# Optimization experiments

Hardware: AMD Instinct MI355X
Metric: run time of the kernel (lower is better)

The kernel has to match this reference:

```python
import jax, jax.numpy as jnp
import numpy as np

NUM_HEADS = 12
HEAD_DIM = 64
SCALE = HEAD_DIM ** -0.5


def setup_inputs() -> dict:
    key = jax.random.key(0)
    k1, k2, k3, k4, k5 = jax.random.split(key, 5)
    B, N, C = 4, 2048, NUM_HEADS * HEAD_DIM
    x = jax.random.normal(k1, (B, N, C), dtype=jnp.float32)
    W_qkv = jax.random.normal(k2, (C, 3 * C), dtype=jnp.float32) * (C ** -0.5)
    b_qkv = jax.random.normal(k3, (3 * C,), dtype=jnp.float32) * 0.02
    W_proj = jax.random.normal(k4, (C, C), dtype=jnp.float32) * (C ** -0.5)
    b_proj = jax.random.normal(k5, (C,), dtype=jnp.float32) * 0.02
    return {"x": x, "W_qkv": W_qkv, "b_qkv": b_qkv, "W_proj": W_proj, "b_proj": b_proj}


def reference(x, W_qkv, b_qkv, W_proj, b_proj):
    B, N, C = x.shape
    H, D = NUM_HEADS, HEAD_DIM
    qkv = x @ W_qkv + b_qkv                      # [B, N, 3C]
    qkv = qkv.reshape(B, N, 3, H, D)
    q = qkv[:, :, 0].transpose(0, 2, 1, 3) * SCALE  # [B, H, N, D]
    k = qkv[:, :, 1].transpose(0, 2, 1, 3)          # [B, H, N, D]
    v = qkv[:, :, 2].transpose(0, 2, 1, 3)          # [B, H, N, D]
    attn = jnp.einsum("bhnd,bhmd->bhnm", q, k)   # [B, H, N, N]
    attn = jax.nn.softmax(attn, axis=-1)
    ctx = jnp.einsum("bhnm,bhmd->bhnd", attn, v)  # [B, H, N, D]
    attn_out = ctx.transpose(0, 2, 1, 3).reshape(B, N, C)
    out = attn_out @ W_proj + b_proj
    return (out, attn_out)
```

## Files before the change

kernel.cpp:

```cpp
#include <hip/hip_runtime.h>
#include <stdint.h>

typedef unsigned short u16;
using bf16x8 = __attribute__((ext_vector_type(8))) __bf16;
using s16x8  = __attribute__((ext_vector_type(8))) short;
using f32x4  = __attribute__((ext_vector_type(4))) float;

#define SCALE_Q 0.125f
#define LOG2E 1.44269504088896f

__device__ __forceinline__ u16 f2bf(float f) {
  union { float f; uint32_t u; } v; v.f = f;
  uint32_t u = v.u;
  return (u16)((u + 0x7FFFu + ((u >> 16) & 1)) >> 16);
}

__device__ __forceinline__ bf16x8 ld_frag(const u16* p) {
  return __builtin_bit_cast(bf16x8, *(const s16x8*)p);
}

__device__ __forceinline__ f32x4 MF(bf16x8 a, bf16x8 b, f32x4 c) {
  return __builtin_amdgcn_mfma_f32_16x16x32_bf16(a, b, c, 0, 0, 0);
}

__device__ __forceinline__ void gld16(const u16* g, u16* l) {
  __builtin_amdgcn_global_load_lds(
      (const __attribute__((address_space(1))) uint32_t*)g,
      (__attribute__((address_space(3))) uint32_t*)l, 16, 0, 0);
}

__device__ __forceinline__ uint32_t pk_bf16(float a, float b) {
  uint32_t u0 = __builtin_bit_cast(uint32_t, a) + 0x8000u;
  uint32_t u1 = __builtin_bit_cast(uint32_t, b) + 0x8000u;
  return __builtin_amdgcn_perm(u1, u0, 0x07060302u);
}

__global__ void cvt_f32_bf16(const float* __restrict__ in, u16* __restrict__ out, int n) {
  int i = (blockIdx.x * 256 + threadIdx.x) * 4;
  if (i < n) {
    float4 v = *(const float4*)(in + i);
    uint2 o;
    o.x = (uint32_t)f2bf(v.x) | ((uint32_t)f2bf(v.y) << 16);
    o.y = (uint32_t)f2bf(v.z) | ((uint32_t)f2bf(v.w) << 16);
    *(uint2*)(out + i) = o;
  }
}

__global__ void transpose_cvt(const float* __restrict__ in, u16* __restrict__ out, int R, int C) {
  __shared__ float tile[32][33];
  int c0 = blockIdx.x * 32, r0 = blockIdx.y * 32;
  int tx = threadIdx.x & 31, ty = threadIdx.x >> 5;
#pragma unroll
  for (int j = 0; j < 32; j += 8)
    tile[ty + j][tx] = in[(size_t)(r0 + ty + j) * C + c0 + tx];
  __syncthreads();
#pragma unroll
  for (int j = 0; j < 32; j += 8)
    out[(size_t)(c0 + ty + j) * R + r0 + tx] = f2bf(tile[tx][ty + j]);
}

template <int MODE>
__global__ __launch_bounds__(256) void gemm_k768(
    const u16* __restrict__ A, const u16* __restrict__ Bt, const float* __restrict__ bias,
    u16* __restrict__ q_out, u16* __restrict__ k_out, u16* __restrict__ v_out,
    float* __restrict__ c_out) {
  constexpr int K = 768;
  __shared__ __align__(16) u16 sA[128 * 64];
  __shared__ __align__(16) u16 sB[128 * 64];
  const int tid = threadIdx.x;
  const int lane = tid & 63, wave = tid >> 6;
  const int ml = lane & 15, kg = lane >> 4;
  const int wr = wave >> 1, wc = wave & 1;
  const int bn = blockIdx.x, bm = blockIdx.y;

  f32x4 acc[4][4] = {};
  const u16* Abase = A + (size_t)(bm * 128) * K;
  const u16* Bbase = Bt + (size_t)(bn * 128) * K;

  for (int k0 = 0; k0 < K; k0 += 64) {
#pragma unroll
    for (int p = 0; p < 4; p++) {
      int q = p * 256 + tid;
      int r = q >> 3, s = q & 7, c = s ^ (r & 7);
      gld16(Abase + (size_t)r * K + k0 + c * 8, sA + q * 8);
      gld16(Bbase + (size_t)r * K + k0 + c * 8, sB + q * 8);
    }
    __syncthreads();
#pragma unroll
    for (int kc = 0; kc < 2; kc++) {
      bf16x8 af[4], bfr[4];
      int ac = kc * 4 + kg;
#pragma unroll
      for (int i = 0; i < 4; i++) {
        int arow = wr * 64 + i * 16 + ml;
        af[i] = ld_frag(sA + (arow * 8 + (ac ^ (arow & 7))) * 8);
        int brow = wc * 64 + i * 16 + ml;
        bfr[i] = ld_frag(sB + (brow * 8 + (ac ^ (brow & 7))) * 8);
      }
#pragma unroll
      for (int mi = 0; mi < 4; mi++)
#pragma unroll
        for (int ni = 0; ni < 4; ni++)
          acc[mi][ni] = MF(af[mi], bfr[ni], acc[mi][ni]);
    }
    __syncthreads();
  }

  if (MODE == 0) {
#pragma unroll
    for (int ni = 0; ni < 4; ni++) {
      int n = bn * 128 + wc * 64 + ni * 16 + ml;
      int s = n / 768, rem = n - s * 768;
      int h = rem >> 6, d = rem & 63;
      float bv = bias[n];
      if (s == 2) {
#pragma unroll
        for (int mi = 0; mi < 4; mi++) {
          int m0 = bm * 128 + wr * 64 + mi * 16 + kg * 4;
          int bi = m0 >> 11, tok = m0 & 2047;
          uint2 o;
          o.x = pk_bf16(acc[mi][ni][0] + bv, acc[mi][ni][1] + bv);
          o.y = pk_bf16(acc[mi][ni][2] + bv, acc[mi][ni][3] + bv);
          *(uint2*)&v_out[((size_t)(bi * 12 + h) * 64 + d) * 2048 + tok] = o;
        }
      } else {
        u16* dst = (s == 0) ? q_out : k_out;
        float scl = (s == 0) ? SCALE_Q * LOG2E : 1.0f;
#pragma unroll
        for (int mi = 0; mi < 4; mi++) {
          int m0 = bm * 128 + wr * 64 + mi * 16 + kg * 4;
#pragma unroll
          for (int r = 0; r < 4; r++) {
            int m = m0 + r;
            int bi = m >> 11, tok = m & 2047;
            dst[(size_t)(bi * 12 + h) * 131072 + (size_t)tok * 64 + d] = f2bf((acc[mi][ni][r] + bv) * scl);
          }
        }
      }
    }
  } else {
#pragma unroll
    for (int ni = 0; ni < 4; ni++) {
      int n = bn * 128 + wc * 64 + ni * 16 + ml;
      float bv = bias[n];
#pragma unroll
      for (int mi = 0; mi < 4; mi++) {
        int m0 = bm * 128 + wr * 64 + mi * 16 + kg * 4;
#pragma unroll
        for (int r = 0; r < 4; r++)
          c_out[(size_t)(m0 + r) * 768 + n] = acc[mi][ni][r] + bv;
      }
    }
  }
}

__global__ __launch_bounds__(256) void gemm_proj(
    const u16* __restrict__ A, const u16* __restrict__ Bt, const float* __restrict__ bias,
    float* __restrict__ c_out) {
  constexpr int K = 768;
  __shared__ __align__(16) u16 sA[128 * 64];
  __shared__ __align__(16) u16 sB[64 * 64];
  const int tid = threadIdx.x;
  const int lane = tid & 63, wave = tid >> 6;
  const int ml = lane & 15, kg = lane >> 4;
  const int bn = blockIdx.x, bm = blockIdx.y;
  f32x4 acc[2][4] = {};
  const u16* Abase = A + (size_t)(bm * 128) * K;
  const u16* Bbase = Bt + (size_t)(bn * 64) * K;

  for (int k0 = 0; k0 < K; k0 += 64) {
#pragma unroll
    for (int p = 0; p < 4; p++) {
      int q = p * 256 + tid;
      int r = q >> 3, s = q & 7, c = s ^ (r & 7);
      gld16(Abase + (size_t)r * K + k0 + c * 8, sA + q * 8);
    }
#pragma unroll
    for (int p = 0; p < 2; p++) {
      int q = p * 256 + tid;
      int r = q >> 3, s = q & 7, c = s ^ (r & 7);
      gld16(Bbase + (size_t)r * K + k0 + c * 8, sB + q * 8);
    }
    __syncthreads();
#pragma unroll
    for (int kc = 0; kc < 2; kc++) {
      int ac = kc * 4 + kg;
      bf16x8 af[2], bfr[4];
#pragma unroll
      for (int i = 0; i < 2; i++) {
        int arow = wave * 32 + i * 16 + ml;
        af[i] = ld_frag(sA + (arow * 8 + (ac ^ (arow & 7))) * 8);
      }
#pragma unroll
      for (int i = 0; i < 4; i++) {
        int brow = i * 16 + ml;
        bfr[i] = ld_frag(sB + (brow * 8 + (ac ^ (brow & 7))) * 8);
      }
#pragma unroll
      for (int mi = 0; mi < 2; mi++)
#pragma unroll
        for (int ni = 0; ni < 4; ni++)
          acc[mi][ni] = MF(af[mi], bfr[ni], acc[mi][ni]);
    }
    __syncthreads();
  }
#pragma unroll
  for (int ni = 0; ni < 4; ni++) {
    int n = bn * 64 + ni * 16 + ml;
    float bv = bias[n];
#pragma unroll
    for (int mi = 0; mi < 2; mi++) {
      int m0 = bm * 128 + wave * 32 + mi * 16 + kg * 4;
#pragma unroll
      for (int r = 0; r < 4; r++)
        c_out[(size_t)(m0 + r) * 768 + n] = acc[mi][ni][r] + bv;
    }
  }
}

__global__ __launch_bounds__(256, 3) void attn_kernel(
    const u16* __restrict__ qs, const u16* __restrict__ ks, const u16* __restrict__ vt,
    float* __restrict__ attn_f32, u16* __restrict__ attn_bf) {
  __shared__ __align__(16) u16 sK[2][64 * 64];
  __shared__ __align__(16) u16 sV[2][64 * 64];
  __shared__ __align__(16) u16 sP[4][32 * 72];
  const int tid = threadIdx.x, lane = tid & 63, wave = tid >> 6;
  const int ml = lane & 15, kg = lane >> 4;
  const int bh = blockIdx.y;
  const int q0 = blockIdx.x * 128 + wave * 32;
  const size_t base = (size_t)bh * 2048 * 64;

  bf16x8 qf[2][2];
#pragma unroll
  for (int qt = 0; qt < 2; qt++) {
    const u16* qp = qs + base + (size_t)(q0 + qt * 16 + ml) * 64 + kg * 8;
    qf[qt][0] = ld_frag(qp);
    qf[qt][1] = ld_frag(qp + 32);
  }
  f32x4 l4[2] = {};
  f32x4 O[2][4] = {};
  u16* myP = sP[wave];

  int buf = 0;
  auto stage = [&](int b, int kt) {
#pragma unroll
    for (int p = 0; p < 2; p++) {
      int q = p * 256 + tid;
      int r = q >> 3, s = q & 7, c = s ^ (r & 7);
      gld16(ks + base + (size_t)(kt + r) * 64 + c * 8, &sK[b][q * 8]);
      gld16(vt + base + (size_t)r * 2048 + kt + c * 8, &sV[b][q * 8]);
    }
  };

  stage(0, 0);
  for (int kt = 0; kt < 2048; kt += 64) {
    __syncthreads();
    if (kt + 64 < 2048) stage(buf ^ 1, kt + 64);

    f32x4 sc[2][4] = {};
#pragma unroll
    for (int nt = 0; nt < 4; nt++) {
#pragma unroll
      for (int kc = 0; kc < 2; kc++) {
        int krow = nt * 16 + ml;
        int c = kc * 4 + kg;
        bf16x8 kf = ld_frag(&sK[buf][(krow * 8 + (c ^ (krow & 7))) * 8]);
        sc[0][nt] = MF(kf, qf[0][kc], sc[0][nt]);
        sc[1][nt] = MF(kf, qf[1][kc], sc[1][nt]);
      }
    }

#pragma unroll
    for (int qt = 0; qt < 2; qt++) {
      u16* rowp = myP + (qt * 16 + ml) * 72;
#pragma unroll
      for (int nt = 0; nt < 4; nt++) {
        f32x4 p;
#pragma unroll
        for (int r = 0; r < 4; r++) p[r] = __builtin_amdgcn_exp2f(sc[qt][nt][r]);
        l4[qt] += p;
        uint2 w;
        w.x = pk_bf16(p[0], p[1]);
        w.y = pk_bf16(p[2], p[3]);
        *(uint2*)(rowp + nt * 16 + kg * 4) = w;
      }
    }

    asm volatile("s_waitcnt lgkmcnt(0)" ::: "memory");

#pragma unroll
    for (int kc = 0; kc < 2; kc++) {
      bf16x8 pf0 = ld_frag(myP + ml * 72 + kc * 32 + kg * 8);
      bf16x8 pf1 = ld_frag(myP + (16 + ml) * 72 + kc * 32 + kg * 8);
#pragma unroll
      for (int nt2 = 0; nt2 < 4; nt2++) {
        int vrow = nt2 * 16 + ml;
        int c = kc * 4 + kg;
        bf16x8 vf = ld_frag(&sV[buf][(vrow * 8 + (c ^ (vrow & 7))) * 8]);
        O[0][nt2] = MF(pf0, vf, O[0][nt2]);
        O[1][nt2] = MF(pf1, vf, O[1][nt2]);
      }
    }
    buf ^= 1;
  }

  float linv[2];
#pragma unroll
  for (int qt = 0; qt < 2; qt++) {
    float s = l4[qt][0] + l4[qt][1] + l4[qt][2] + l4[qt][3];
    s += __shfl_xor(s, 16);
    s += __shfl_xor(s, 32);
    linv[qt] = __builtin_amdgcn_rcpf(s);
  }
  int b = bh / 12, h = bh - b * 12;
#pragma unroll
  for (int qt = 0; qt < 2; qt++)
#pragma unroll
    for (int r = 0; r < 4; r++) {
      float inv = __shfl(linv[qt], kg * 4 + r, 64);
      int qrow = q0 + qt * 16 + kg * 4 + r;
      size_t rowoff = ((size_t)(b * 2048 + qrow)) * 768 + h * 64;
#pragma unroll
      for (int nt2 = 0; nt2 < 4; nt2++) {
        float v = O[qt][nt2][r] * inv;
        int d = nt2 * 16 + ml;
        attn_f32[rowoff + d] = v;
        attn_bf[rowoff + d] = f2bf(v);
      }
    }
}

extern "C" void kernel_launch(void* const* d_in, const int* in_sizes, int n_in,
                              void* d_out, int out_size, void* d_ws, size_t ws_size,
                              hipStream_t stream) {
  const float* x      = (const float*)d_in[0];
  const float* W_qkv  = (const float*)d_in[1];
  const float* b_qkv  = (const float*)d_in[2];
  const float* W_proj = (const float*)d_in[3];
  const float* b_proj = (const float*)d_in[4];
  float* out      = (float*)d_out;
  float* attn_out = out + (size_t)8192 * 768;

  char* ws = (char*)d_ws;
  const size_t SZ_XB = (size_t)8192 * 768 * 2;
  u16* xb      = (u16*)(ws);
  u16* wqkv_t  = (u16*)(ws + SZ_XB);
  u16* wproj_t = (u16*)(ws + SZ_XB + 3538944);
  u16* qs      = (u16*)(ws + SZ_XB + 3538944 + 1179648);
  u16* ks      = (u16*)((char*)qs + SZ_XB);
  u16* vt      = (u16*)((char*)ks + SZ_XB);
  u16* ab      = xb;

  cvt_f32_bf16<<<6144, 256, 0, stream>>>(x, xb, 8192 * 768);
  transpose_cvt<<<dim3(2304 / 32, 768 / 32), 256, 0, stream>>>(W_qkv, wqkv_t, 768, 2304);
  transpose_cvt<<<dim3(768 / 32, 768 / 32), 256, 0, stream>>>(W_proj, wproj_t, 768, 768);
  gemm_k768<0><<<dim3(2304 / 128, 8192 / 128), 256, 0, stream>>>(
      xb, wqkv_t, b_qkv, qs, ks, vt, nullptr);
  attn_kernel<<<dim3(16, 48), 256, 0, stream>>>(qs, ks, vt, attn_out, ab);
  gemm_proj<<<dim3(12, 64), 256, 0, stream>>>(ab, wproj_t, b_proj, out);
}
```

Before: 231.5 us.

## Keep P in registers for PV MFMA and stage V-transpose stores through LDS

The attention kernel drops the per-wave LDS round trip for the softmax probabilities. It packs P directly into registers and computes O^T with the 16x16x16 bf16 MFMA, using V^T fragments as the A operand, so the output lands row-contiguous and can be written with vectorized float4/uint2 stores. The QKV GEMM epilogue for V blocks now transposes through shared memory so the V^T output is written with 16-byte row-contiguous stores instead of scattered 8-byte ones. The trade is more, smaller MFMAs (16x16x16 instead of 16x16x32) in exchange for removing the LDS write/wait/read traffic and uncoalesced epilogue stores.

```diff
diff --git a/kernel.cpp b/kernel.cpp
--- a/kernel.cpp
+++ b/kernel.cpp
@@ -4,6 +4,7 @@
 typedef unsigned short u16;
 using bf16x8 = __attribute__((ext_vector_type(8))) __bf16;
 using s16x8  = __attribute__((ext_vector_type(8))) short;
+using s16x4  = __attribute__((ext_vector_type(4))) short;
 using f32x4  = __attribute__((ext_vector_type(4))) float;
 
 #define SCALE_Q 0.125f
@@ -21,6 +22,9 @@
 
 __device__ __forceinline__ f32x4 MF(bf16x8 a, bf16x8 b, f32x4 c) {
   return __builtin_amdgcn_mfma_f32_16x16x32_bf16(a, b, c, 0, 0, 0);
+}
+__device__ __forceinline__ f32x4 MF16(s16x4 a, s16x4 b, f32x4 c) {
+  return __builtin_amdgcn_mfma_f32_16x16x16bf16_1k(a, b, c, 0, 0, 0);
 }
 
 __device__ __forceinline__ void gld16(const u16* g, u16* l) {
@@ -59,14 +63,13 @@
     out[(size_t)(c0 + ty + j) * R + r0 + tx] = f2bf(tile[tx][ty + j]);
 }
 
-template <int MODE>
-__global__ __launch_bounds__(256) void gemm_k768(
+__global__ __launch_bounds__(256) void gemm_qkv(
     const u16* __restrict__ A, const u16* __restrict__ Bt, const float* __restrict__ bias,
-    u16* __restrict__ q_out, u16* __restrict__ k_out, u16* __restrict__ v_out,
-    float* __restrict__ c_out) {
+    u16* __restrict__ q_out, u16* __restrict__ k_out, u16* __restrict__ v_out) {
   constexpr int K = 768;
-  __shared__ __align__(16) u16 sA[128 * 64];
-  __shared__ __align__(16) u16 sB[128 * 64];
+  __shared__ __align__(16) u16 smem[17408];
+  u16* sA = smem;
+  u16* sB = smem + 8192;
   const int tid = threadIdx.x;
   const int lane = tid & 63, wave = tid >> 6;
   const int ml = lane & 15, kg = lane >> 4;
@@ -106,49 +109,48 @@
     __syncthreads();
   }
 
-  if (MODE == 0) {
+  if (bn >= 12) {
+    uint32_t* t32 = (uint32_t*)smem;
+#pragma unroll
+    for (int ni = 0; ni < 4; ni++) {
+      int n_local = wc * 64 + ni * 16 + ml;
+      float bv = bias[bn * 128 + n_local];
+#pragma unroll
+      for (int mi = 0; mi < 4; mi++) {
+        int mh = wr * 32 + mi * 8 + kg * 2;
+        t32[n_local * 68 + mh]     = pk_bf16(acc[mi][ni][0] + bv, acc[mi][ni][1] + bv);
+        t32[n_local * 68 + mh + 1] = pk_bf16(acc[mi][ni][2] + bv, acc[mi][ni][3] + bv);
+      }
+    }
+    __syncthreads();
+    int row = tid >> 1, seg = tid & 1;
+    int dg = (bn - 12) * 128 + row;
+    int h = dg >> 6, d = dg & 63;
+    int bi = bm >> 4, tok0 = (bm & 15) * 128;
+    u16* dst = v_out + ((size_t)(bi * 12 + h) * 64 + d) * 2048 + tok0 + seg * 64;
+    const uint32_t* src = t32 + row * 68 + seg * 32;
+#pragma unroll
+    for (int j = 0; j < 8; j++)
+      *(uint4*)(dst + j * 8) = *(const uint4*)(src + j * 4);
+  } else {
 #pragma unroll
     for (int ni = 0; ni < 4; ni++) {
       int n = bn * 128 + wc * 64 + ni * 16 + ml;
-      int s = n / 768, rem = n - s * 768;
+      int s = n >> 9 >= 1 ? (n >= 768 ? 1 : 0) : 0;
+      int rem = n - s * 768;
       int h = rem >> 6, d = rem & 63;
       float bv = bias[n];
-      if (s == 2) {
-#pragma unroll
-        for (int mi = 0; mi < 4; mi++) {
-          int m0 = bm * 128 + wr * 64 + mi * 16 + kg * 4;
-          int bi = m0 >> 11, tok = m0 & 2047;
-          uint2 o;
-          o.x = pk_bf16(acc[mi][ni][0] + bv, acc[mi][ni][1] + bv);
-          o.y = pk_bf16(acc[mi][ni][2] + bv, acc[mi][ni][3] + bv);
-          *(uint2*)&v_out[((size_t)(bi * 12 + h) * 64 + d) * 2048 + tok] = o;
-        }
-      } else {
-        u16* dst = (s == 0) ? q_out : k_out;
-        float scl = (s == 0) ? SCALE_Q * LOG2E : 1.0f;
-#pragma unroll
-        for (int mi = 0; mi < 4; mi++) {
-          int m0 = bm * 128 + wr * 64 + mi * 16 + kg * 4;
-#pragma unroll
-          for (int r = 0; r < 4; r++) {
-            int m = m0 + r;
-            int bi = m >> 11, tok = m & 2047;
-            dst[(size_t)(bi * 12 + h) * 131072 + (size_t)tok * 64 + d] = f2bf((acc[mi][ni][r] + bv) * scl);
-          }
-        }
-      }
-    }
-  } else {
-#pragma unroll
-    for (int ni = 0; ni < 4; ni++) {
-      int n = bn * 128 + wc * 64 + ni * 16 + ml;
-      float bv = bias[n];
+      u16* dst = (s == 0) ? q_out : k_out;
+      float scl = (s == 0) ? SCALE_Q * LOG2E : 1.0f;
 #pragma unroll
       for (int mi = 0; mi < 4; mi++) {
         int m0 = bm * 128 + wr * 64 + mi * 16 + kg * 4;
 #pragma unroll
-        for (int r = 0; r < 4; r++)
-          c_out[(size_t)(m0 + r) * 768 + n] = acc[mi][ni][r] + bv;
+        for (int r = 0; r < 4; r++) {
+          int m = m0 + r;
+          int bi = m >> 11, tok = m & 2047;
+          dst[(size_t)(bi * 12 + h) * 131072 + (size_t)tok * 64 + d] = f2bf((acc[mi][ni][r] + bv) * scl);
+        }
       }
     }
   }
@@ -223,7 +225,6 @@
     float* __restrict__ attn_f32, u16* __restrict__ attn_bf) {
   __shared__ __align__(16) u16 sK[2][64 * 64];
   __shared__ __align__(16) u16 sV[2][64 * 64];
-  __shared__ __align__(16) u16 sP[4][32 * 72];
   const int tid = threadIdx.x, lane = tid & 63, wave = tid >> 6;
   const int ml = lane & 15, kg = lane >> 4;
   const int bh = blockIdx.y;
@@ -239,7 +240,6 @@
   }
   f32x4 l4[2] = {};
   f32x4 O[2][4] = {};
-  u16* myP = sP[wave];
 
   int buf = 0;
   auto stage = [&](int b, int kt) {
@@ -270,9 +270,9 @@
       }
     }
 
-#pragma unroll
-    for (int qt = 0; qt < 2; qt++) {
-      u16* rowp = myP + (qt * 16 + ml) * 72;
+    s16x4 pb[2][4];
+#pragma unroll
+    for (int qt = 0; qt < 2; qt++)
 #pragma unroll
       for (int nt = 0; nt < 4; nt++) {
         f32x4 p;
@@ -282,52 +282,44 @@
         uint2 w;
         w.x = pk_bf16(p[0], p[1]);
         w.y = pk_bf16(p[2], p[3]);
-        *(uint2*)(rowp + nt * 16 + kg * 4) = w;
-      }
-    }
-
-    asm volatile("s_waitcnt lgkmcnt(0)" ::: "memory");
-
-#pragma unroll
-    for (int kc = 0; kc < 2; kc++) {
-      bf16x8 pf0 = ld_frag(myP + ml * 72 + kc * 32 + kg * 8);
-      bf16x8 pf1 = ld_frag(myP + (16 + ml) * 72 + kc * 32 + kg * 8);
-#pragma unroll
-      for (int nt2 = 0; nt2 < 4; nt2++) {
-        int vrow = nt2 * 16 + ml;
-        int c = kc * 4 + kg;
-        bf16x8 vf = ld_frag(&sV[buf][(vrow * 8 + (c ^ (vrow & 7))) * 8]);
-        O[0][nt2] = MF(pf0, vf, O[0][nt2]);
-        O[1][nt2] = MF(pf1, vf, O[1][nt2]);
+        pb[qt][nt] = __builtin_bit_cast(s16x4, w);
+      }
+
+#pragma unroll
+    for (int dt = 0; dt < 4; dt++) {
+      int r = dt * 16 + ml;
+#pragma unroll
+      for (int kc4 = 0; kc4 < 4; kc4++) {
+        int c0 = kc4 * 2 + (kg >> 1);
+        s16x4 vf = *(const s16x4*)(&sV[buf][((r * 8 + (c0 ^ (r & 7))) * 8 + (kg & 1) * 4)]);
+        O[0][dt] = MF16(vf, pb[0][kc4], O[0][dt]);
+        O[1][dt] = MF16(vf, pb[1][kc4], O[1][dt]);
       }
     }
     buf ^= 1;
   }
 
-  float linv[2];
+  int b = bh / 12, h = bh - b * 12;
 #pragma unroll
   for (int qt = 0; qt < 2; qt++) {
     float s = l4[qt][0] + l4[qt][1] + l4[qt][2] + l4[qt][3];
     s += __shfl_xor(s, 16);
     s += __shfl_xor(s, 32);
-    linv[qt] = __builtin_amdgcn_rcpf(s);
-  }
-  int b = bh / 12, h = bh - b * 12;
-#pragma unroll
-  for (int qt = 0; qt < 2; qt++)
-#pragma unroll
-    for (int r = 0; r < 4; r++) {
-      float inv = __shfl(linv[qt], kg * 4 + r, 64);
-      int qrow = q0 + qt * 16 + kg * 4 + r;
-      size_t rowoff = ((size_t)(b * 2048 + qrow)) * 768 + h * 64;
-#pragma unroll
-      for (int nt2 = 0; nt2 < 4; nt2++) {
-        float v = O[qt][nt2][r] * inv;
-        int d = nt2 * 16 + ml;
-        attn_f32[rowoff + d] = v;
-        attn_bf[rowoff + d] = f2bf(v);
-      }
-    }
+    float inv = __builtin_amdgcn_rcpf(s);
+    int qrow = q0 + qt * 16 + ml;
+    size_t rowoff = ((size_t)(b * 2048 + qrow)) * 768 + h * 64;
+#pragma unroll
+    for (int dt = 0; dt < 4; dt++) {
+      f32x4 v = O[qt][dt];
+      float4 o4 = {v[0] * inv, v[1] * inv, v[2] * inv, v[3] * inv};
+      int d0 = dt * 16 + kg * 4;
+      *(float4*)(attn_f32 + rowoff + d0) = o4;
+      uint2 w;
+      w.x = pk_bf16(o4.x, o4.y);
+      w.y = pk_bf16(o4.z, o4.w);
+      *(uint2*)(attn_bf + rowoff + d0) = w;
+    }
+  }
 }
 
 extern "C" void kernel_launch(void* const* d_in, const int* in_sizes, int n_in,
@@ -354,8 +346,7 @@
   cvt_f32_bf16<<<6144, 256, 0, stream>>>(x, xb, 8192 * 768);
   transpose_cvt<<<dim3(2304 / 32, 768 / 32), 256, 0, stream>>>(W_qkv, wqkv_t, 768, 2304);
   transpose_cvt<<<dim3(768 / 32, 768 / 32), 256, 0, stream>>>(W_proj, wproj_t, 768, 768);
-  gemm_k768<0><<<dim3(2304 / 128, 8192 / 128), 256, 0, stream>>>(
-      xb, wqkv_t, b_qkv, qs, ks, vt, nullptr);
+  gemm_qkv<<<dim3(18, 64), 256, 0, stream>>>(xb, wqkv_t, b_qkv, qs, ks, vt);
   attn_kernel<<<dim3(16, 48), 256, 0, stream>>>(qs, ks, vt, attn_out, ab);
   gemm_proj<<<dim3(12, 64), 256, 0, stream>>>(ab, wproj_t, b_proj, out);
 }
```

Result: slower. 236.5 us (+2.1%).
